# Optimization experiments

Measured on AMD Instinct MI355X. Metric: run time of the kernel, lower is better.

## Reference

```python
import jax, jax.numpy as jnp
import numpy as np

B, N, K, DIMS, F_DIMS = 2, 32768, 16, 2, 32
DS, DH, DO = 32, 32, 32
DA = DS + DH                      # 64
CH = (DIMS + 1) * (1 + K) + DIMS  # 53
CONV_IN = DIMS + (1 + K) * DA     # 1090
CONV_OUT = (1 + K) * DO           # 544


def setup_inputs() -> dict:
    key = jax.random.key(0)
    ks = jax.random.split(key, 6)
    s = 0.05
    return {
        "pc": jax.random.normal(ks[0], (B, N, 1 + K, DIMS), jnp.float32),
        "feats": jax.random.normal(ks[1], (B, N, 1 + K, F_DIMS), jnp.float32),
        "W_mlp": jax.random.normal(ks[2], (CH, DS), jnp.float32) * s,
        "b_mlp": jnp.zeros((DS,), jnp.float32),
        "W_att": jax.random.normal(ks[3], (DA, DA), jnp.float32) * s,
        "b_att": jnp.zeros((DA,), jnp.float32),
        "W_conv": jax.random.normal(ks[4], (CONV_IN, CONV_OUT), jnp.float32) * s,
        "b_conv": jnp.zeros((CONV_OUT,), jnp.float32),
        "W_skip": jax.random.normal(ks[5], (DO + F_DIMS, DO), jnp.float32) * s,
        "b_skip": jnp.zeros((DO,), jnp.float32),
    }


def reference(pc, feats, W_mlp, b_mlp, W_att, b_att, W_conv, b_conv, W_skip, b_skip):
    # ---- LocSE: relative-position encoding ----
    # rpbn_i[b,n,j] = concat(pc[b,n,i] - pc[b,n,j], ||pc[b,n,j]||)
    norms = jnp.linalg.norm(pc, axis=-1, keepdims=True)          # (B,N,1+K,1)
    # diffs[b,n,j,i,:] = pc[b,n,i,:] - pc[b,n,j,:]
    diffs = pc[:, :, None, :, :] - pc[:, :, :, None, :]          # (B,N,1+K,1+K,dims)
    norms_b = jnp.broadcast_to(norms[:, :, :, None, :], diffs.shape[:-1] + (1,))
    blocks = jnp.concatenate([diffs, norms_b], axis=-1)          # (B,N,1+K,1+K,dims+1)
    blocks = blocks.reshape(pc.shape[:3] + ((1 + K) * (DIMS + 1),))
    rppe = jnp.concatenate([pc, blocks], axis=-1)                # (B,N,1+K,CH)
    r = jax.nn.relu(rppe @ W_mlp + b_mlp)                        # (B,N,1+K,DS)
    se = jnp.concatenate([r, feats], axis=-1)                    # (B,N,1+K,DA)

    # ---- attention pooling (softmax over channel axis) ----
    att = jax.nn.softmax(se @ W_att + b_att, axis=-1) * se       # (B,N,1+K,DA)
    reshaped = att.reshape(att.shape[0], att.shape[1], (1 + K) * DA)

    cat = jnp.concatenate([pc[:, :, 0], reshaped], axis=-1)      # (B,N,CONV_IN)
    res = jax.nn.relu(cat @ W_conv + b_conv)                     # (B,N,(1+K)*DO)
    res = res.reshape(res.shape[0], res.shape[1], 1 + K, DO)

    skip_in = jnp.concatenate([feats, res], axis=-1)             # (B,N,1+K,F+DO)
    skip = jax.nn.relu(skip_in @ W_skip + b_skip)                # (B,N,1+K,DO)
    return skip
```

## Files before the change

kernel.cpp:

```cpp
#include <hip/hip_runtime.h>
#include <hip/hip_bf16.h>
#include <cstdint>

#define KNB      17
#define CH       53
#define MP       16
#define BM       64
#define NTHR     512
#define NRT      17
#define SE_LD    72
#define CATW     1120
#define RES_LD   552

#define NE_CONV  (35*34*512)
#define NE_MLP   (2*2*512)
#define NE_ATT   (2*4*512)
#define NE_SKIP  (2*2*512)
#define WS_MLP   (NE_CONV)
#define WS_ATT   (WS_MLP + NE_MLP)
#define WS_SKIP  (WS_ATT + NE_ATT)
#define WS_TOTAL (WS_SKIP + NE_SKIP)

typedef __bf16 bf16x8 __attribute__((ext_vector_type(8)));
typedef float  f32x4  __attribute__((ext_vector_type(4)));
typedef unsigned short u16x4 __attribute__((ext_vector_type(4)));
typedef unsigned short u16x8 __attribute__((ext_vector_type(8)));

__device__ __forceinline__ unsigned short f2b(float f) {
    union { __bf16 h; unsigned short u; } v; v.h = (__bf16)f; return v.u;
}
__device__ __forceinline__ float b2f(unsigned short b) {
    union { unsigned u; float f; } v; v.u = ((unsigned)b) << 16;
    return v.f;
}

__global__ void seac_prep(const float* __restrict__ Wmlp, const float* __restrict__ Watt,
                          const float* __restrict__ Wconv, const float* __restrict__ Wskip,
                          unsigned short* __restrict__ ws)
{
    int i = blockIdx.x * 256 + threadIdx.x;
    if (i >= WS_TOTAL) return;
    float v;
    if (i < WS_MLP) {
        int idx = i;
        int jj = idx & 7, l = (idx >> 3) & 63, t = idx >> 9;
        int nt = t % 34, ks = t / 34;
        int k = 32*ks + 8*(l >> 4) + jj;
        int o = 16*nt + (l & 15);
        int ok;
        if (k < 1088)       ok = k + 2;
        else if (k == 1088) ok = 0;
        else if (k == 1089) ok = 1;
        else                ok = -1;
        v = (ok >= 0) ? Wconv[ok*544 + o] : 0.f;
    } else if (i < WS_ATT) {
        int idx = i - WS_MLP;
        int jj = idx & 7, l = (idx >> 3) & 63, t = idx >> 9;
        int nt = t & 1, ks = t >> 1;
        int k = 32*ks + 8*(l >> 4) + jj;
        int o = 16*nt + (l & 15);
        v = (k < CH) ? Wmlp[k*32 + o] : 0.f;
    } else if (i < WS_SKIP) {
        int idx = i - WS_ATT;
        int jj = idx & 7, l = (idx >> 3) & 63, t = idx >> 9;
        int nt = t & 3, ks = t >> 2;
        int k = 32*ks + 8*(l >> 4) + jj;
        int o = 16*nt + (l & 15);
        v = Watt[k*64 + o];
    } else {
        int idx = i - WS_SKIP;
        int jj = idx & 7, l = (idx >> 3) & 63, t = idx >> 9;
        int nt = t & 1, ks = t >> 1;
        int k = 32*ks + 8*(l >> 4) + jj;
        int o = 16*nt + (l & 15);
        v = Wskip[k*32 + o];
    }
    ws[i] = f2b(v);
}

__global__ __launch_bounds__(NTHR, 6) void seac_locse(
    const float* __restrict__ pc, const float* __restrict__ feats,
    const float* __restrict__ bmlp, const float* __restrict__ batt,
    const unsigned short* __restrict__ ws, unsigned short* __restrict__ catg,
    int pt0)
{
    __shared__ unsigned short se_l[272 * SE_LD];
    __shared__ float pcl[MP][KNB][2];
    __shared__ float bmlp_l[32];
    __shared__ float batt_l[64];

    const int tid  = threadIdx.x;
    const int w    = tid >> 6;
    const int l    = tid & 63;
    const int g    = l >> 4;
    const int c15  = l & 15;
    const long pbase = (long)pt0 + (long)blockIdx.x * MP;
    const bf16x8* wsB8 = (const bf16x8*)ws;

    if (tid < MP*KNB) {
        int p = tid / KNB, i = tid - p*KNB;
        float x = pc[(pbase + p)*(KNB*2) + 2*i];
        float y = pc[(pbase + p)*(KNB*2) + 2*i + 1];
        pcl[p][i][0] = x; pcl[p][i][1] = y;
    }
    for (int q = tid; q < MP*544/4; q += NTHR) {
        float4 f = *(const float4*)&feats[pbase*544 + 4*q];
        int e0 = 4*q; int p = e0 / 544; int rem = e0 - 544*p;
        int j = rem >> 5, c = rem & 31;
        u16x4 u; u[0] = f2b(f.x); u[1] = f2b(f.y); u[2] = f2b(f.z); u[3] = f2b(f.w);
        *(u16x4*)&se_l[(p*KNB + j)*SE_LD + 32 + c] = u;
    }
    if (tid < 32)                     bmlp_l[tid]      = bmlp[tid];
    else if (tid >= 64 && tid < 128)  batt_l[tid-64]   = batt[tid-64];
    __syncthreads();

    {
        bf16x8 Bm[2][2];
        #pragma unroll
        for (int ks = 0; ks < 2; ++ks)
            #pragma unroll
            for (int nt = 0; nt < 2; ++nt)
                Bm[ks][nt] = wsB8[(WS_MLP >> 3) + (ks*2 + nt)*64 + l];
        float bch[2][4];
        #pragma unroll
        for (int nt = 0; nt < 2; ++nt)
            #pragma unroll
            for (int r = 0; r < 4; ++r) bch[nt][r] = bmlp_l[16*nt + 4*g + r];

        for (int mt = w; mt < NRT; mt += 8) {
            int row = 16*mt + c15;
            int p = row / KNB, j = row - p*KNB;
            float pjx = pcl[p][j][0], pjy = pcl[p][j][1];
            float nj = sqrtf(pjx*pjx + pjy*pjy);
            f32x4 acc0 = {0.f,0.f,0.f,0.f}, acc1 = {0.f,0.f,0.f,0.f};
            #pragma unroll
            for (int ks = 0; ks < 2; ++ks) {
                union { unsigned short u[8]; bf16x8 v; } a;
                #pragma unroll
                for (int jj = 0; jj < 8; ++jj) {
                    int k = 32*ks + 8*g + jj;
                    float vv;
                    if (k == 0) vv = pjx;
                    else if (k == 1) vv = pjy;
                    else if (k < CH) {
                        int kk = k - 2, ii = kk/3, t3 = kk - 3*ii;
                        vv = (t3 == 0) ? (pcl[p][ii][0] - pjx)
                           : (t3 == 1) ? (pcl[p][ii][1] - pjy) : nj;
                    } else vv = 0.f;
                    a.u[jj] = f2b(vv);
                }
                acc0 = __builtin_amdgcn_mfma_f32_16x16x32_bf16(Bm[ks][0], a.v, acc0, 0, 0, 0);
                acc1 = __builtin_amdgcn_mfma_f32_16x16x32_bf16(Bm[ks][1], a.v, acc1, 0, 0, 0);
            }
            u16x4 o0, o1;
            #pragma unroll
            for (int r = 0; r < 4; ++r) {
                o0[r] = f2b(fmaxf(acc0[r] + bch[0][r], 0.f));
                o1[r] = f2b(fmaxf(acc1[r] + bch[1][r], 0.f));
            }
            *(u16x4*)&se_l[row*SE_LD + 4*g]      = o0;
            *(u16x4*)&se_l[row*SE_LD + 16 + 4*g] = o1;
        }
    }
    __syncthreads();

    {
        bf16x8 Ba[2][4];
        #pragma unroll
        for (int ks = 0; ks < 2; ++ks)
            #pragma unroll
            for (int nt = 0; nt < 4; ++nt)
                Ba[ks][nt] = wsB8[(WS_ATT >> 3) + (ks*4 + nt)*64 + l];
        float bch[16];
        #pragma unroll
        for (int nt = 0; nt < 4; ++nt)
            #pragma unroll
            for (int r = 0; r < 4; ++r) bch[4*nt+r] = batt_l[16*nt + 4*g + r];

        for (int mt = w; mt < NRT; mt += 8) {
            int row = 16*mt + c15;
            bf16x8 b0 = *(const bf16x8*)&se_l[row*SE_LD + 8*g];
            bf16x8 b1 = *(const bf16x8*)&se_l[row*SE_LD + 32 + 8*g];
            f32x4 acc[4];
            #pragma unroll
            for (int nt = 0; nt < 4; ++nt) {
                f32x4 z = {0.f,0.f,0.f,0.f};
                acc[nt] = __builtin_amdgcn_mfma_f32_16x16x32_bf16(Ba[0][nt], b0, z,       0, 0, 0);
                acc[nt] = __builtin_amdgcn_mfma_f32_16x16x32_bf16(Ba[1][nt], b1, acc[nt], 0, 0, 0);
            }
            float vv[16];
            #pragma unroll
            for (int nt = 0; nt < 4; ++nt)
                #pragma unroll
                for (int r = 0; r < 4; ++r) vv[4*nt+r] = acc[nt][r] + bch[4*nt+r];
            float m = vv[0];
            #pragma unroll
            for (int i = 1; i < 16; ++i) m = fmaxf(m, vv[i]);
            m = fmaxf(m, __shfl_xor(m, 16)); m = fmaxf(m, __shfl_xor(m, 32));
            float s = 0.f;
            #pragma unroll
            for (int i = 0; i < 16; ++i) { vv[i] = __expf(vv[i] - m); s += vv[i]; }
            s += __shfl_xor(s, 16); s += __shfl_xor(s, 32);
            float inv = 1.f / s;
            #pragma unroll
            for (int nt = 0; nt < 4; ++nt) {
                u16x4 sv = *(const u16x4*)&se_l[row*SE_LD + 16*nt + 4*g];
                u16x4 ov;
                #pragma unroll
                for (int r = 0; r < 4; ++r) ov[r] = f2b(vv[4*nt+r]*inv * b2f(sv[r]));
                *(u16x4*)&se_l[row*SE_LD + 16*nt + 4*g] = ov;
            }
        }
    }
    __syncthreads();

    for (int c = tid; c < MP*140; c += NTHR) {
        int p = c / 140, rem = c - 140*p;
        int e = 8*rem;
        u16x8 v;
        if (e < 1088) {
            int row = p*KNB + (e >> 6), col = e & 63;
            v = *(const u16x8*)&se_l[row*SE_LD + col];
        } else {
            #pragma unroll
            for (int q = 0; q < 8; ++q) v[q] = 0;
            if (e == 1088) { v[0] = f2b(pcl[p][0][0]); v[1] = f2b(pcl[p][0][1]); }
        }
        *(u16x8*)&catg[(pbase + p)*CATW + e] = v;
    }
}

__global__ __launch_bounds__(NTHR, 4) void seac_conv(
    const unsigned short* __restrict__ catg, const float* __restrict__ feats,
    const float* __restrict__ bconv, const float* __restrict__ bskip,
    const unsigned short* __restrict__ ws, float* __restrict__ out, int pt0)
{
    __shared__ unsigned short res_l[BM * RES_LD];
    __shared__ float bconv_l[544];

    const int tid  = threadIdx.x;
    const int w    = tid >> 6;
    const int l    = tid & 63;
    const int g    = l >> 4;
    const int c15  = l & 15;
    const long pbase = (long)pt0 + (long)blockIdx.x * BM;
    const bf16x8* wsB8 = (const bf16x8*)ws;

    for (int i = tid; i < 544; i += NTHR) bconv_l[i] = bconv[i];
    __syncthreads();

    const bf16x8* arow[4];
    #pragma unroll
    for (int mt = 0; mt < 4; ++mt)
        arow[mt] = (const bf16x8*)&catg[(pbase + 16*mt + c15)*CATW + 8*g];

    f32x4 acc[4][5];
    #pragma unroll
    for (int mt = 0; mt < 4; ++mt)
        #pragma unroll
        for (int t = 0; t < 5; ++t) { f32x4 z = {0.f,0.f,0.f,0.f}; acc[mt][t] = z; }

    for (int ks = 0; ks < 35; ++ks) {
        bf16x8 a[4];
        #pragma unroll
        for (int mt = 0; mt < 4; ++mt) a[mt] = arow[mt][4*ks];
        #pragma unroll
        for (int t = 0; t < 5; ++t) {
            int nt = w + 8*t;
            if (nt < 34) {
                bf16x8 b = wsB8[(ks*34 + nt)*64 + l];
                #pragma unroll
                for (int mt = 0; mt < 4; ++mt)
                    acc[mt][t] = __builtin_amdgcn_mfma_f32_16x16x32_bf16(a[mt], b, acc[mt][t], 0, 0, 0);
            }
        }
    }

    #pragma unroll
    for (int t = 0; t < 5; ++t) {
        int nt = w + 8*t;
        if (nt < 34) {
            float bc = bconv_l[16*nt + c15];
            #pragma unroll
            for (int mt = 0; mt < 4; ++mt)
                #pragma unroll
                for (int r = 0; r < 4; ++r)
                    res_l[(16*mt + 4*g + r)*RES_LD + 16*nt + c15] =
                        f2b(fmaxf(acc[mt][t][r] + bc, 0.f));
        }
    }
    __syncthreads();

    {
        bf16x8 Bs[2][2];
        #pragma unroll
        for (int ks = 0; ks < 2; ++ks)
            #pragma unroll
            for (int nt = 0; nt < 2; ++nt)
                Bs[ks][nt] = wsB8[(WS_SKIP >> 3) + (ks*2 + nt)*64 + l];
        float bs0 = bskip[c15], bs1 = bskip[16 + c15];

        for (int tt = 0; tt < 9; ++tt) {
            int mt2 = w + 8*tt;
            if (mt2 < 68) {
                int rr = 16*mt2 + c15;
                int pp = rr / 17, jn = rr - 17*pp;
                float4 f0 = *(const float4*)&feats[(pbase*KNB + rr)*32 + 8*g];
                float4 f1 = *(const float4*)&feats[(pbase*KNB + rr)*32 + 8*g + 4];
                union { unsigned short u[8]; bf16x8 v; } af;
                af.u[0]=f2b(f0.x); af.u[1]=f2b(f0.y); af.u[2]=f2b(f0.z); af.u[3]=f2b(f0.w);
                af.u[4]=f2b(f1.x); af.u[5]=f2b(f1.y); af.u[6]=f2b(f1.z); af.u[7]=f2b(f1.w);
                bf16x8 ar = *(const bf16x8*)&res_l[pp*RES_LD + 32*jn + 8*g];
                f32x4 z = {0.f,0.f,0.f,0.f};
                f32x4 a0 = __builtin_amdgcn_mfma_f32_16x16x32_bf16(af.v, Bs[0][0], z, 0, 0, 0);
                a0       = __builtin_amdgcn_mfma_f32_16x16x32_bf16(ar,   Bs[1][0], a0, 0, 0, 0);
                f32x4 a1 = __builtin_amdgcn_mfma_f32_16x16x32_bf16(af.v, Bs[0][1], z, 0, 0, 0);
                a1       = __builtin_amdgcn_mfma_f32_16x16x32_bf16(ar,   Bs[1][1], a1, 0, 0, 0);
                #pragma unroll
                for (int r = 0; r < 4; ++r) {
                    long orow = pbase*KNB + 16*mt2 + 4*g + r;
                    out[orow*32 + c15]      = fmaxf(a0[r] + bs0, 0.f);
                    out[orow*32 + 16 + c15] = fmaxf(a1[r] + bs1, 0.f);
                }
            }
        }
    }
}

extern "C" void kernel_launch(void* const* d_in, const int* in_sizes, int n_in,
                              void* d_out, int out_size, void* d_ws, size_t ws_size,
                              hipStream_t stream)
{
    const float* pc    = (const float*)d_in[0];
    const float* feats = (const float*)d_in[1];
    const float* Wmlp  = (const float*)d_in[2];
    const float* bmlp  = (const float*)d_in[3];
    const float* Watt  = (const float*)d_in[4];
    const float* batt  = (const float*)d_in[5];
    const float* Wconv = (const float*)d_in[6];
    const float* bconv = (const float*)d_in[7];
    const float* Wskip = (const float*)d_in[8];
    const float* bskip = (const float*)d_in[9];
    float* out = (float*)d_out;
    unsigned short* ws16 = (unsigned short*)d_ws;

    int npts = in_sizes[0] / (KNB*2);

    size_t frag_bytes = (size_t)WS_TOTAL * 2;
    size_t cat_off    = (frag_bytes + 255) & ~(size_t)255;
    unsigned short* catg = (unsigned short*)((char*)d_ws + cat_off);
    size_t avail = (ws_size > cat_off) ? (ws_size - cat_off) : 0;
    long maxpts = (long)(avail / (CATW * 2));
    long chunk  = (maxpts / BM) * BM;
    if (chunk > npts) chunk = npts;
    if (chunk < BM)   chunk = BM;

    int prep_blocks = (WS_TOTAL + 255) / 256;
    hipLaunchKernelGGL(seac_prep, dim3(prep_blocks), dim3(256), 0, stream,
                       Wmlp, Watt, Wconv, Wskip, ws16);

    for (long base = 0; base < npts; base += chunk) {
        long c = npts - base; if (c > chunk) c = chunk;
        hipLaunchKernelGGL(seac_locse, dim3((int)(c / MP)), dim3(NTHR), 0, stream,
                           pc, feats, bmlp, batt, ws16, catg, (int)base);
        hipLaunchKernelGGL(seac_conv, dim3((int)(c / BM)), dim3(NTHR), 0, stream,
                           catg, feats, bconv, bskip, ws16, out, (int)base);
    }
}
```

Measured before the change: 349.0 us.

## Store concat activations in MFMA fragment order for coalesced conv loads

The locse kernel now writes the bf16 concat buffer pre-swizzled into 64-point groups. The layout matches the A-operand fragment order of the 16x16x32 MFMA, so the conv kernel reads contiguous 1KB per wavefront through a single advancing pointer instead of strided per-row loads. The K loop is also unrolled by 5. The cost moves to the locse store pattern, which now scatters 16-byte writes within each group.

```diff
diff --git a/kernel.cpp b/kernel.cpp
--- a/kernel.cpp
+++ b/kernel.cpp
@@ -9,8 +9,9 @@
 #define NTHR     512
 #define NRT      17
 #define SE_LD    72
-#define CATW     1120
 #define RES_LD   552
+
+#define CATT_GRP 71680
 
 #define NE_CONV  (35*34*512)
 #define NE_MLP   (2*2*512)
@@ -81,7 +82,7 @@
 __global__ __launch_bounds__(NTHR, 6) void seac_locse(
     const float* __restrict__ pc, const float* __restrict__ feats,
     const float* __restrict__ bmlp, const float* __restrict__ batt,
-    const unsigned short* __restrict__ ws, unsigned short* __restrict__ catg,
+    const unsigned short* __restrict__ ws, unsigned short* __restrict__ catT,
     int pt0)
 {
     __shared__ unsigned short se_l[272 * SE_LD];
@@ -214,24 +215,30 @@
     }
     __syncthreads();
 
-    for (int c = tid; c < MP*140; c += NTHR) {
-        int p = c / 140, rem = c - 140*p;
-        int e = 8*rem;
-        u16x8 v;
-        if (e < 1088) {
-            int row = p*KNB + (e >> 6), col = e & 63;
-            v = *(const u16x8*)&se_l[row*SE_LD + col];
-        } else {
-            #pragma unroll
-            for (int q = 0; q < 8; ++q) v[q] = 0;
-            if (e == 1088) { v[0] = f2b(pcl[p][0][0]); v[1] = f2b(pcl[p][0][1]); }
-        }
-        *(u16x8*)&catg[(pbase + p)*CATW + e] = v;
+    {
+        const int q    = (int)((pbase >> 4) & 3);
+        const long grp = pbase >> 6;
+        unsigned short* dst = catT + grp*CATT_GRP + q*512;
+        for (int idx = tid; idx < 35*64; idx += NTHR) {
+            int ks = idx >> 6, ll = idx & 63;
+            int p = ll & 15, g = ll >> 4;
+            int k0 = 32*ks + 8*g;
+            u16x8 v;
+            if (k0 < 1088) {
+                int row = p*KNB + (k0 >> 6), col = k0 & 63;
+                v = *(const u16x8*)&se_l[row*SE_LD + col];
+            } else {
+                #pragma unroll
+                for (int z = 0; z < 8; ++z) v[z] = 0;
+                if (k0 == 1088) { v[0] = f2b(pcl[p][0][0]); v[1] = f2b(pcl[p][0][1]); }
+            }
+            *(u16x8*)&dst[ks*2048 + ll*8] = v;
+        }
     }
 }
 
 __global__ __launch_bounds__(NTHR, 4) void seac_conv(
-    const unsigned short* __restrict__ catg, const float* __restrict__ feats,
+    const unsigned short* __restrict__ catT, const float* __restrict__ feats,
     const float* __restrict__ bconv, const float* __restrict__ bskip,
     const unsigned short* __restrict__ ws, float* __restrict__ out, int pt0)
 {
@@ -249,10 +256,8 @@
     for (int i = tid; i < 544; i += NTHR) bconv_l[i] = bconv[i];
     __syncthreads();
 
-    const bf16x8* arow[4];
-    #pragma unroll
-    for (int mt = 0; mt < 4; ++mt)
-        arow[mt] = (const bf16x8*)&catg[(pbase + 16*mt + c15)*CATW + 8*g];
+    const long grp = pbase >> 6;
+    const bf16x8* ap = (const bf16x8*)catT + grp*(CATT_GRP/8) + l;
 
     f32x4 acc[4][5];
     #pragma unroll
@@ -260,10 +265,11 @@
         #pragma unroll
         for (int t = 0; t < 5; ++t) { f32x4 z = {0.f,0.f,0.f,0.f}; acc[mt][t] = z; }
 
+    #pragma unroll 5
     for (int ks = 0; ks < 35; ++ks) {
         bf16x8 a[4];
         #pragma unroll
-        for (int mt = 0; mt < 4; ++mt) a[mt] = arow[mt][4*ks];
+        for (int mt = 0; mt < 4; ++mt) a[mt] = ap[mt*64];
         #pragma unroll
         for (int t = 0; t < 5; ++t) {
             int nt = w + 8*t;
@@ -274,6 +280,7 @@
                     acc[mt][t] = __builtin_amdgcn_mfma_f32_16x16x32_bf16(a[mt], b, acc[mt][t], 0, 0, 0);
             }
         }
+        ap += 256;
     }
 
     #pragma unroll
@@ -348,9 +355,9 @@
 
     size_t frag_bytes = (size_t)WS_TOTAL * 2;
     size_t cat_off    = (frag_bytes + 255) & ~(size_t)255;
-    unsigned short* catg = (unsigned short*)((char*)d_ws + cat_off);
+    unsigned short* catT = (unsigned short*)((char*)d_ws + cat_off);
     size_t avail = (ws_size > cat_off) ? (ws_size - cat_off) : 0;
-    long maxpts = (long)(avail / (CATW * 2));
+    long maxpts = (long)(avail / 2240);
     long chunk  = (maxpts / BM) * BM;
     if (chunk > npts) chunk = npts;
     if (chunk < BM)   chunk = BM;
@@ -362,8 +369,8 @@
     for (long base = 0; base < npts; base += chunk) {
         long c = npts - base; if (c > chunk) c = chunk;
         hipLaunchKernelGGL(seac_locse, dim3((int)(c / MP)), dim3(NTHR), 0, stream,
-                           pc, feats, bmlp, batt, ws16, catg, (int)base);
+                           pc, feats, bmlp, batt, ws16, catT, (int)base);
         hipLaunchKernelGGL(seac_conv, dim3((int)(c / BM)), dim3(NTHR), 0, stream,
-                           catg, feats, bconv, bskip, ws16, out, (int)base);
-    }
-}
+                           catT, feats, bconv, bskip, ws16, out, (int)base);
+    }
+}
```

Measured after the change: 446.9 us. 28.0% more time.

## Stage conv A-tiles through LDS with async global_load_lds ring, halve res buffer

Applied to the files above, without the earlier changes.

The conv GEMM's A operand (cat rows) was read straight from global into registers each k-step. It is now prefetched three steps ahead into a 4-slot LDS ring using global_load_lds, with a vmcnt wait and a barrier per step, so global latency overlaps the MFMAs. The epilogue splits the 64-row residual buffer into two 32-row halves to cut LDS use, which may allow more blocks per CU. The cost is a workgroup barrier in every k-iteration and an extra sync between halves.

```diff
diff --git a/kernel.cpp b/kernel.cpp
--- a/kernel.cpp
+++ b/kernel.cpp
@@ -32,6 +32,11 @@
 __device__ __forceinline__ float b2f(unsigned short b) {
     union { unsigned u; float f; } v; v.u = ((unsigned)b) << 16;
     return v.f;
+}
+__device__ __forceinline__ void gload_lds16(const void* g, void* l) {
+    __builtin_amdgcn_global_load_lds(
+        (const __attribute__((address_space(1))) unsigned int*)g,
+        (__attribute__((address_space(3))) unsigned int*)l, 16, 0, 0);
 }
 
 __global__ void seac_prep(const float* __restrict__ Wmlp, const float* __restrict__ Watt,
@@ -235,7 +240,8 @@
     const float* __restrict__ bconv, const float* __restrict__ bskip,
     const unsigned short* __restrict__ ws, float* __restrict__ out, int pt0)
 {
-    __shared__ unsigned short res_l[BM * RES_LD];
+    __shared__ unsigned short astage[4][BM][32];
+    __shared__ unsigned short res_l[32 * RES_LD];
     __shared__ float bconv_l[544];
 
     const int tid  = threadIdx.x;
@@ -247,12 +253,13 @@
     const bf16x8* wsB8 = (const bf16x8*)ws;
 
     for (int i = tid; i < 544; i += NTHR) bconv_l[i] = bconv[i];
-    __syncthreads();
-
-    const bf16x8* arow[4];
-    #pragma unroll
-    for (int mt = 0; mt < 4; ++mt)
-        arow[mt] = (const bf16x8*)&catg[(pbase + 16*mt + c15)*CATW + 8*g];
+
+    if (tid < 256) {
+        const unsigned short* g0 = &catg[(pbase + (tid >> 2))*CATW + 8*(tid & 3)];
+        gload_lds16(g0,      &astage[0][16*(tid >> 6)][0]);
+        gload_lds16(g0 + 32, &astage[1][16*(tid >> 6)][0]);
+        gload_lds16(g0 + 64, &astage[2][16*(tid >> 6)][0]);
+    }
 
     f32x4 acc[4][5];
     #pragma unroll
@@ -261,9 +268,13 @@
         for (int t = 0; t < 5; ++t) { f32x4 z = {0.f,0.f,0.f,0.f}; acc[mt][t] = z; }
 
     for (int ks = 0; ks < 35; ++ks) {
+        asm volatile("s_waitcnt vmcnt(2)" ::: "memory");
+        __builtin_amdgcn_s_barrier();
+        __builtin_amdgcn_sched_barrier(0);
         bf16x8 a[4];
         #pragma unroll
-        for (int mt = 0; mt < 4; ++mt) a[mt] = arow[mt][4*ks];
+        for (int mt = 0; mt < 4; ++mt)
+            a[mt] = *(const bf16x8*)&astage[ks & 3][16*mt + c15][8*g];
         #pragma unroll
         for (int t = 0; t < 5; ++t) {
             int nt = w + 8*t;
@@ -274,39 +285,47 @@
                     acc[mt][t] = __builtin_amdgcn_mfma_f32_16x16x32_bf16(a[mt], b, acc[mt][t], 0, 0, 0);
             }
         }
-    }
-
+        if (ks + 3 < 35 && tid < 256)
+            gload_lds16(&catg[(pbase + (tid >> 2))*CATW + 32*(ks+3) + 8*(tid & 3)],
+                        &astage[(ks+3) & 3][16*(tid >> 6)][0]);
+    }
+    __syncthreads();
+
+    bf16x8 Bs[2][2];
     #pragma unroll
-    for (int t = 0; t < 5; ++t) {
-        int nt = w + 8*t;
-        if (nt < 34) {
-            float bc = bconv_l[16*nt + c15];
-            #pragma unroll
-            for (int mt = 0; mt < 4; ++mt)
-                #pragma unroll
-                for (int r = 0; r < 4; ++r)
-                    res_l[(16*mt + 4*g + r)*RES_LD + 16*nt + c15] =
-                        f2b(fmaxf(acc[mt][t][r] + bc, 0.f));
-        }
-    }
-    __syncthreads();
-
-    {
-        bf16x8 Bs[2][2];
-        #pragma unroll
-        for (int ks = 0; ks < 2; ++ks)
-            #pragma unroll
-            for (int nt = 0; nt < 2; ++nt)
-                Bs[ks][nt] = wsB8[(WS_SKIP >> 3) + (ks*2 + nt)*64 + l];
-        float bs0 = bskip[c15], bs1 = bskip[16 + c15];
-
-        for (int tt = 0; tt < 9; ++tt) {
+    for (int ks = 0; ks < 2; ++ks)
+        #pragma unroll
+        for (int nt = 0; nt < 2; ++nt)
+            Bs[ks][nt] = wsB8[(WS_SKIP >> 3) + (ks*2 + nt)*64 + l];
+    float bs0 = bskip[c15], bs1 = bskip[16 + c15];
+
+    #pragma unroll
+    for (int half = 0; half < 2; ++half) {
+        #pragma unroll
+        for (int t = 0; t < 5; ++t) {
+            int nt = w + 8*t;
+            if (nt < 34) {
+                float bc = bconv_l[16*nt + c15];
+                #pragma unroll
+                for (int mh = 0; mh < 2; ++mh) {
+                    int mt = 2*half + mh;
+                    #pragma unroll
+                    for (int r = 0; r < 4; ++r)
+                        res_l[(16*mh + 4*g + r)*RES_LD + 16*nt + c15] =
+                            f2b(fmaxf(acc[mt][t][r] + bc, 0.f));
+                }
+            }
+        }
+        __syncthreads();
+
+        const long gofs = pbase*KNB + 544*half;
+        for (int tt = 0; tt < 5; ++tt) {
             int mt2 = w + 8*tt;
-            if (mt2 < 68) {
+            if (mt2 < 34) {
                 int rr = 16*mt2 + c15;
                 int pp = rr / 17, jn = rr - 17*pp;
-                float4 f0 = *(const float4*)&feats[(pbase*KNB + rr)*32 + 8*g];
-                float4 f1 = *(const float4*)&feats[(pbase*KNB + rr)*32 + 8*g + 4];
+                float4 f0 = *(const float4*)&feats[(gofs + rr)*32 + 8*g];
+                float4 f1 = *(const float4*)&feats[(gofs + rr)*32 + 8*g + 4];
                 union { unsigned short u[8]; bf16x8 v; } af;
                 af.u[0]=f2b(f0.x); af.u[1]=f2b(f0.y); af.u[2]=f2b(f0.z); af.u[3]=f2b(f0.w);
                 af.u[4]=f2b(f1.x); af.u[5]=f2b(f1.y); af.u[6]=f2b(f1.z); af.u[7]=f2b(f1.w);
@@ -318,12 +337,13 @@
                 a1       = __builtin_amdgcn_mfma_f32_16x16x32_bf16(ar,   Bs[1][1], a1, 0, 0, 0);
                 #pragma unroll
                 for (int r = 0; r < 4; ++r) {
-                    long orow = pbase*KNB + 16*mt2 + 4*g + r;
+                    long orow = gofs + 16*mt2 + 4*g + r;
                     out[orow*32 + c15]      = fmaxf(a0[r] + bs0, 0.f);
                     out[orow*32 + 16 + c15] = fmaxf(a1[r] + bs1, 0.f);
                 }
             }
         }
+        if (half == 0) __syncthreads();
     }
 }
 
```

Result: faster. 316.6 us (-9.3%).
